# Performance work log

Hardware: AMD Instinct MI355X
Metric: run time of the kernel (lower is better)

## Reference

```python
import jax, jax.numpy as jnp
import numpy as np

KAPPA = 5.0
EPS_NORM = 1e-12  # torch F.normalize eps
EPS_LOG = 1e-09


def setup_inputs() -> dict:
    key = jax.random.key(0)
    student_output = jax.random.normal(key, (16384, 256), dtype=jnp.float32)
    return {"student_output": student_output}


def reference(student_output) -> jnp.ndarray:
    # L2-normalize rows (matches F.normalize: x / max(||x||, eps))
    norm = jnp.linalg.norm(student_output, axis=-1, keepdims=True)
    x_norm = student_output / jnp.maximum(norm, EPS_NORM)
    # pairwise cosine similarity [n, n]
    sim = x_norm @ x_norm.T
    kernel = jnp.exp(KAPPA * sim)
    density_estimates = kernel.sum(axis=1)  # [n]
    entropy = -jnp.mean(jnp.log(density_estimates + EPS_LOG))
    return entropy
```

## Files before the change

### kernel.cpp

```cpp
#include <hip/hip_runtime.h>


#define NROWS 16384
#define KDIM 256
#define NTILE 128
#define NT (NROWS / NTILE)
#define NSTRIP 4
#define TOTAL_BLOCKS (NT * NSTRIP)

#define SQRT_KLOG2E 2.68579577857f

typedef int i32x4_t __attribute__((ext_vector_type(4)));
typedef int i32x8_t __attribute__((ext_vector_type(8)));
typedef float f32x16_t __attribute__((ext_vector_type(16)));
typedef __attribute__((address_space(1))) const void global_cvoid_t;
typedef __attribute__((address_space(3))) void lds_void_t;

#if __has_builtin(__builtin_amdgcn_exp2f)
#define EXP2(x) __builtin_amdgcn_exp2f(x)
#else
#define EXP2(x) exp2f(x)
#endif

union frag8 { i32x8_t v8; i32x4_t v4[2]; };

__global__ __launch_bounds__(256)
void kde_normalize(const float* __restrict__ X, unsigned int* __restrict__ Xn8,
                   float* __restrict__ density, unsigned int* __restrict__ ticket) {
  const int wave = threadIdx.x >> 6;
  const int lane = threadIdx.x & 63;
  const int row = blockIdx.x * 4 + wave;
  const float4 v = ((const float4*)(X + (size_t)row * KDIM))[lane];
  float ss = v.x * v.x + v.y * v.y + v.z * v.z + v.w * v.w;
  ss += __shfl_xor(ss, 1);
  ss += __shfl_xor(ss, 2);
  ss += __shfl_xor(ss, 4);
  ss += __shfl_xor(ss, 8);
  ss += __shfl_xor(ss, 16);
  ss += __shfl_xor(ss, 32);
  const float scale = SQRT_KLOG2E / fmaxf(sqrtf(ss), 1e-12f);
  int p = 0;
  p = __builtin_amdgcn_cvt_pk_fp8_f32(v.x * scale, v.y * scale, p, false);
  p = __builtin_amdgcn_cvt_pk_fp8_f32(v.z * scale, v.w * scale, p, true);
  Xn8[(size_t)row * 64 + lane] = (unsigned int)p;
  if (threadIdx.x < 4) density[blockIdx.x * 4 + threadIdx.x] = 0.0f;
  if (blockIdx.x == 0 && threadIdx.x == 0) *ticket = 0u;
}

__global__ __launch_bounds__(512, 4)
void kde_gemm(const unsigned char* __restrict__ Xn8, float* __restrict__ density,
              unsigned int* __restrict__ ticket, float* __restrict__ out) {
  extern __shared__ char smem[];
  char* buf0 = smem;
  char* buf1 = smem + 32768;

  const int tid = threadIdx.x;
  const int wave = tid >> 6;
  const int lane = tid & 63;
  const int wr = wave >> 1;
  const int wc = wave & 1;
  const int m32 = lane & 31;
  const int h = lane >> 5;
  const int bi = blockIdx.x;
  const int s = blockIdx.y;
  const int t0 = s * 16;
  const int nt = (s == 0 && bi < NT / 2) ? 17 : 16;
  const char* Xb = (const char*)Xn8;

#define STAGE(base_row, dst)                                                      \
  for (int c = wave; c < 32; c += 8) {                                            \
    const int rt = c >> 3, kb = (c >> 1) & 3, hh = c & 1;                         \
    const size_t gofs =                                                           \
        (size_t)((base_row) + rt * 32 + m32) * KDIM + kb * 64 + h * 32 + hh * 16; \
    __builtin_amdgcn_global_load_lds((global_cvoid_t*)(Xb + gofs),                \
                                     (lds_void_t*)((dst) + c * 1024), 16, 0, 0);  \
  }

  STAGE(bi * NTILE, buf0);
  STAGE(((bi + t0) & (NT - 1)) * NTILE, buf1);
  __syncthreads();

  frag8 areg[4];
#pragma unroll
  for (int kb = 0; kb < 4; kb++) {
    const char* pa = buf0 + (wr * 8 + kb * 2) * 1024 + lane * 16;
    areg[kb].v4[0] = *(const i32x4_t*)pa;
    areg[kb].v4[1] = *(const i32x4_t*)(pa + 1024);
  }
  __syncthreads();

  float rs[16];
#pragma unroll
  for (int r = 0; r < 16; r++) rs[r] = 0.0f;

  for (int k = 0; k < nt; ++k) {
    const int t = t0 + (k == 16 ? 48 : k) + (k == 16 ? 16 : 0);
    const int J = (bi + t) & (NT - 1);
    char* rbuf = (k & 1) ? buf0 : buf1;
    char* sbuf = (k & 1) ? buf1 : buf0;

    if (k + 1 < nt) {
      const int tn = t0 + (k + 1 == 16 ? 64 : k + 1);
      STAGE(((bi + tn) & (NT - 1)) * NTILE, sbuf);
    }

    f32x16_t acc[2];
#pragma unroll
    for (int j = 0; j < 2; j++) acc[j] = (f32x16_t)0.0f;

#pragma unroll
    for (int kb = 0; kb < 4; ++kb) {
      frag8 bf[2];
#pragma unroll
      for (int j = 0; j < 2; j++) {
        const char* pb = rbuf + ((wc * 2 + j) * 8 + kb * 2) * 1024 + lane * 16;
        bf[j].v4[0] = *(const i32x4_t*)pb;
        bf[j].v4[1] = *(const i32x4_t*)(pb + 1024);
      }
#pragma unroll
      for (int j = 0; j < 2; j++)
        acc[j] = __builtin_amdgcn_mfma_scale_f32_32x32x64_f8f6f4(
            areg[kb].v8, bf[j].v8, acc[j], 0, 0, 0, 127, 0, 127);
    }

    float cs[2] = {0.0f, 0.0f};
#pragma unroll
    for (int j = 0; j < 2; j++)
#pragma unroll
      for (int r = 0; r < 16; r++) {
        const float e = EXP2(acc[j][r]);
        rs[r] += e;
        cs[j] += e;
      }

    if (t != 0) {
#pragma unroll
      for (int j = 0; j < 2; j++) {
        float v = cs[j] + __shfl_xor(cs[j], 32);
        if (h == 0)
          atomicAdd(&density[J * NTILE + wc * 64 + j * 32 + m32], v);
      }
    }

    __syncthreads();
  }

#pragma unroll
  for (int r = 0; r < 16; r++) {
    float v = rs[r];
    v += __shfl_xor(v, 1);
    v += __shfl_xor(v, 2);
    v += __shfl_xor(v, 4);
    v += __shfl_xor(v, 8);
    v += __shfl_xor(v, 16);
    if (m32 == 0) {
      const int row = bi * NTILE + wr * 32 + (r & 3) + 8 * (r >> 2) + 4 * h;
      atomicAdd(&density[row], v);
    }
  }
#undef STAGE

  __syncthreads();
  if (tid == 0) {
    __threadfence();
    ((volatile unsigned int*)smem)[0] = atomicAdd(ticket, 1u);
  }
  __syncthreads();
  if (((volatile unsigned int*)smem)[0] == TOTAL_BLOCKS - 1) {
    __threadfence();
    float ssum = 0.0f;
    for (int i = tid; i < NROWS; i += 512) {
      const float d = __hip_atomic_load(&density[i], __ATOMIC_RELAXED,
                                        __HIP_MEMORY_SCOPE_AGENT);
      ssum += logf(d + 1e-9f);
    }
    ssum += __shfl_xor(ssum, 1);
    ssum += __shfl_xor(ssum, 2);
    ssum += __shfl_xor(ssum, 4);
    ssum += __shfl_xor(ssum, 8);
    ssum += __shfl_xor(ssum, 16);
    ssum += __shfl_xor(ssum, 32);
    float* red = ((float*)smem) + 16;
    if (lane == 0) red[wave] = ssum;
    __syncthreads();
    if (tid == 0) {
      float tot = 0.0f;
      for (int w = 0; w < 8; w++) tot += red[w];
      out[0] = -tot / (float)NROWS;
    }
  }
}

extern "C" void kernel_launch(void* const* d_in, const int* in_sizes, int n_in,
                              void* d_out, int out_size, void* d_ws, size_t ws_size,
                              hipStream_t stream) {
  const float* X = (const float*)d_in[0];
  float* out = (float*)d_out;
  char* ws = (char*)d_ws;
  unsigned int* Xn8 = (unsigned int*)ws;
  float* density = (float*)(ws + (size_t)NROWS * KDIM);
  unsigned int* ticket = (unsigned int*)(density + NROWS);

  hipFuncSetAttribute((const void*)kde_gemm,
                      hipFuncAttributeMaxDynamicSharedMemorySize, 65536);

  kde_normalize<<<NROWS / 4, 256, 0, stream>>>(X, Xn8, density, ticket);
  kde_gemm<<<dim3(NT, NSTRIP), 512, 65536, stream>>>((const unsigned char*)ws,
                                                     density, ticket, out);
}
```

Baseline: 124.5 us.

## Defer column-sum atomics to an LDS-reduced epilogue and fully unroll tile loop

Per-tile column sums are now stored in registers and written to LDS after the main loop. They are reduced across the four row-waves there, so each column gets one global atomicAdd instead of four per tile. The main 16-tile loop is fully unrolled, and the extra diagonal-symmetric tile is peeled into its own block. This cuts global atomic traffic and keeps atomics out of the pipelined MFMA loop, in exchange for more registers and a larger code body.

Result: slower. 355.5 us (+185.6%).

```diff
diff --git a/kernel.cpp b/kernel.cpp
--- a/kernel.cpp
+++ b/kernel.cpp
@@ -64,7 +64,7 @@
   const int bi = blockIdx.x;
   const int s = blockIdx.y;
   const int t0 = s * 16;
-  const int nt = (s == 0 && bi < NT / 2) ? 17 : 16;
+  const bool extra = (s == 0 && bi < NT / 2);
   const char* Xb = (const char*)Xn8;
 
 #define STAGE(base_row, dst)                                                      \
@@ -92,17 +92,20 @@
   float rs[16];
 #pragma unroll
   for (int r = 0; r < 16; r++) rs[r] = 0.0f;
-
-  for (int k = 0; k < nt; ++k) {
-    const int t = t0 + (k == 16 ? 48 : k) + (k == 16 ? 16 : 0);
-    const int J = (bi + t) & (NT - 1);
+  float cs_save[16];
+
+#pragma unroll
+  for (int k = 0; k < 16; ++k) {
+    const int J = (bi + t0 + k) & (NT - 1);
     char* rbuf = (k & 1) ? buf0 : buf1;
     char* sbuf = (k & 1) ? buf1 : buf0;
 
-    if (k + 1 < nt) {
-      const int tn = t0 + (k + 1 == 16 ? 64 : k + 1);
-      STAGE(((bi + tn) & (NT - 1)) * NTILE, sbuf);
-    }
+    if (k < 15) {
+      STAGE(((bi + t0 + k + 1) & (NT - 1)) * NTILE, sbuf);
+    } else if (extra) {
+      STAGE(((bi + 64) & (NT - 1)) * NTILE, sbuf);
+    }
+    (void)J;
 
     f32x16_t acc[2];
 #pragma unroll
@@ -123,26 +126,77 @@
             areg[kb].v8, bf[j].v8, acc[j], 0, 0, 0, 127, 0, 127);
     }
 
-    float cs[2] = {0.0f, 0.0f};
-#pragma unroll
-    for (int j = 0; j < 2; j++)
-#pragma unroll
-      for (int r = 0; r < 16; r++) {
-        const float e = EXP2(acc[j][r]);
-        rs[r] += e;
-        cs[j] += e;
+    float c0 = 0.0f, c1 = 0.0f;
+#pragma unroll
+    for (int r = 0; r < 16; r++) {
+      const float e0 = EXP2(acc[0][r]);
+      const float e1 = EXP2(acc[1][r]);
+      rs[r] += e0 + e1;
+      c0 += e0;
+      c1 += e1;
+    }
+    c0 += __shfl_xor(c0, 32);
+    c1 += __shfl_xor(c1, 32);
+    cs_save[k] = h ? c1 : c0;
+
+    __syncthreads();
+  }
+
+  if (extra) {
+    const int J = (bi + 64) & (NT - 1);
+    f32x16_t acc[2];
+#pragma unroll
+    for (int j = 0; j < 2; j++) acc[j] = (f32x16_t)0.0f;
+#pragma unroll
+    for (int kb = 0; kb < 4; ++kb) {
+      frag8 bf[2];
+#pragma unroll
+      for (int j = 0; j < 2; j++) {
+        const char* pb = buf1 + ((wc * 2 + j) * 8 + kb * 2) * 1024 + lane * 16;
+        bf[j].v4[0] = *(const i32x4_t*)pb;
+        bf[j].v4[1] = *(const i32x4_t*)(pb + 1024);
       }
-
-    if (t != 0) {
-#pragma unroll
-      for (int j = 0; j < 2; j++) {
-        float v = cs[j] + __shfl_xor(cs[j], 32);
-        if (h == 0)
-          atomicAdd(&density[J * NTILE + wc * 64 + j * 32 + m32], v);
+#pragma unroll
+      for (int j = 0; j < 2; j++)
+        acc[j] = __builtin_amdgcn_mfma_scale_f32_32x32x64_f8f6f4(
+            areg[kb].v8, bf[j].v8, acc[j], 0, 0, 0, 127, 0, 127);
+    }
+    float c0 = 0.0f, c1 = 0.0f;
+#pragma unroll
+    for (int r = 0; r < 16; r++) {
+      const float e0 = EXP2(acc[0][r]);
+      const float e1 = EXP2(acc[1][r]);
+      rs[r] += e0 + e1;
+      c0 += e0;
+      c1 += e1;
+    }
+    c0 += __shfl_xor(c0, 32);
+    c1 += __shfl_xor(c1, 32);
+    if (h == 0) {
+      atomicAdd(&density[J * NTILE + wc * 64 + m32], c0);
+      atomicAdd(&density[J * NTILE + wc * 64 + 32 + m32], c1);
+    }
+  }
+
+  {
+    float* csLds = (float*)buf0;
+#pragma unroll
+    for (int k = 0; k < 16; ++k)
+      csLds[(wr * 16 + k) * 128 + wc * 64 + lane] = cs_save[k];
+    __syncthreads();
+#pragma unroll
+    for (int i = 0; i < 4; ++i) {
+      const int idx = tid + i * 512;
+      const int k = idx >> 7, col = idx & 127;
+      if (s != 0 || k != 0) {
+        const float v = csLds[(0 * 16 + k) * 128 + col] +
+                        csLds[(1 * 16 + k) * 128 + col] +
+                        csLds[(2 * 16 + k) * 128 + col] +
+                        csLds[(3 * 16 + k) * 128 + col];
+        const int J = (bi + t0 + k) & (NT - 1);
+        atomicAdd(&density[J * NTILE + col], v);
       }
     }
-
-    __syncthreads();
   }
 
 #pragma unroll
```

## Drop LDS double buffering and double grid strips for more occupancy

Applied to the files above, without the earlier changes.

Removes the double-buffered LDS prefetch so each block uses 32 KB instead of 64 KB, and stages each column tile synchronously before computing. NSTRIP goes from 4 to 8, doubling the block count and halving the tiles per block (8 or 9 instead of 16 or 17). The aim is more resident blocks and more parallelism so other blocks hide load latency, replacing in-block overlap. The cost is that each block now stalls on its own loads, and the extra blocks add more atomics and more A-tile reloads. The exp accumulation loop is also reordered to interleave the two accumulators.

Measured after the change: 142.5 us. 14.5% more time.

```diff
diff --git a/kernel.cpp b/kernel.cpp
--- a/kernel.cpp
+++ b/kernel.cpp
@@ -5,7 +5,7 @@
 #define KDIM 256
 #define NTILE 128
 #define NT (NROWS / NTILE)
-#define NSTRIP 4
+#define NSTRIP 8
 #define TOTAL_BLOCKS (NT * NSTRIP)
 
 #define SQRT_KLOG2E 2.68579577857f
@@ -51,8 +51,7 @@
 void kde_gemm(const unsigned char* __restrict__ Xn8, float* __restrict__ density,
               unsigned int* __restrict__ ticket, float* __restrict__ out) {
   extern __shared__ char smem[];
-  char* buf0 = smem;
-  char* buf1 = smem + 32768;
+  char* buf = smem;
 
   const int tid = threadIdx.x;
   const int wave = tid >> 6;
@@ -63,27 +62,25 @@
   const int h = lane >> 5;
   const int bi = blockIdx.x;
   const int s = blockIdx.y;
-  const int t0 = s * 16;
-  const int nt = (s == 0 && bi < NT / 2) ? 17 : 16;
+  const int t0 = s * 8;
+  const int nt = (s == 0 && bi < NT / 2) ? 9 : 8;
   const char* Xb = (const char*)Xn8;
 
-#define STAGE(base_row, dst)                                                      \
+#define STAGE(base_row)                                                           \
   for (int c = wave; c < 32; c += 8) {                                            \
     const int rt = c >> 3, kb = (c >> 1) & 3, hh = c & 1;                         \
     const size_t gofs =                                                           \
         (size_t)((base_row) + rt * 32 + m32) * KDIM + kb * 64 + h * 32 + hh * 16; \
     __builtin_amdgcn_global_load_lds((global_cvoid_t*)(Xb + gofs),                \
-                                     (lds_void_t*)((dst) + c * 1024), 16, 0, 0);  \
-  }
-
-  STAGE(bi * NTILE, buf0);
-  STAGE(((bi + t0) & (NT - 1)) * NTILE, buf1);
-  __syncthreads();
-
+                                     (lds_void_t*)(buf + c * 1024), 16, 0, 0);    \
+  }
+
+  STAGE(bi * NTILE);
+  __syncthreads();
   frag8 areg[4];
 #pragma unroll
   for (int kb = 0; kb < 4; kb++) {
-    const char* pa = buf0 + (wr * 8 + kb * 2) * 1024 + lane * 16;
+    const char* pa = buf + (wr * 8 + kb * 2) * 1024 + lane * 16;
     areg[kb].v4[0] = *(const i32x4_t*)pa;
     areg[kb].v4[1] = *(const i32x4_t*)(pa + 1024);
   }
@@ -94,15 +91,11 @@
   for (int r = 0; r < 16; r++) rs[r] = 0.0f;
 
   for (int k = 0; k < nt; ++k) {
-    const int t = t0 + (k == 16 ? 48 : k) + (k == 16 ? 16 : 0);
+    const int t = (k == 8) ? 64 : t0 + k;
     const int J = (bi + t) & (NT - 1);
-    char* rbuf = (k & 1) ? buf0 : buf1;
-    char* sbuf = (k & 1) ? buf1 : buf0;
-
-    if (k + 1 < nt) {
-      const int tn = t0 + (k + 1 == 16 ? 64 : k + 1);
-      STAGE(((bi + tn) & (NT - 1)) * NTILE, sbuf);
-    }
+
+    STAGE(J * NTILE);
+    __syncthreads();
 
     f32x16_t acc[2];
 #pragma unroll
@@ -113,7 +106,7 @@
       frag8 bf[2];
 #pragma unroll
       for (int j = 0; j < 2; j++) {
-        const char* pb = rbuf + ((wc * 2 + j) * 8 + kb * 2) * 1024 + lane * 16;
+        const char* pb = buf + ((wc * 2 + j) * 8 + kb * 2) * 1024 + lane * 16;
         bf[j].v4[0] = *(const i32x4_t*)pb;
         bf[j].v4[1] = *(const i32x4_t*)(pb + 1024);
       }
@@ -123,22 +116,22 @@
             areg[kb].v8, bf[j].v8, acc[j], 0, 0, 0, 127, 0, 127);
     }
 
-    float cs[2] = {0.0f, 0.0f};
-#pragma unroll
-    for (int j = 0; j < 2; j++)
-#pragma unroll
-      for (int r = 0; r < 16; r++) {
-        const float e = EXP2(acc[j][r]);
-        rs[r] += e;
-        cs[j] += e;
-      }
+    float c0 = 0.0f, c1 = 0.0f;
+#pragma unroll
+    for (int r = 0; r < 16; r++) {
+      const float e0 = EXP2(acc[0][r]);
+      const float e1 = EXP2(acc[1][r]);
+      rs[r] += e0 + e1;
+      c0 += e0;
+      c1 += e1;
+    }
 
     if (t != 0) {
-#pragma unroll
-      for (int j = 0; j < 2; j++) {
-        float v = cs[j] + __shfl_xor(cs[j], 32);
-        if (h == 0)
-          atomicAdd(&density[J * NTILE + wc * 64 + j * 32 + m32], v);
+      c0 += __shfl_xor(c0, 32);
+      c1 += __shfl_xor(c1, 32);
+      if (h == 0) {
+        atomicAdd(&density[J * NTILE + wc * 64 + m32], c0);
+        atomicAdd(&density[J * NTILE + wc * 64 + 32 + m32], c1);
       }
     }
 
@@ -202,9 +195,9 @@
   unsigned int* ticket = (unsigned int*)(density + NROWS);
 
   hipFuncSetAttribute((const void*)kde_gemm,
-                      hipFuncAttributeMaxDynamicSharedMemorySize, 65536);
+                      hipFuncAttributeMaxDynamicSharedMemorySize, 32768);
 
   kde_normalize<<<NROWS / 4, 256, 0, stream>>>(X, Xn8, density, ticket);
-  kde_gemm<<<dim3(NT, NSTRIP), 512, 65536, stream>>>((const unsigned char*)ws,
+  kde_gemm<<<dim3(NT, NSTRIP), 512, 32768, stream>>>((const unsigned char*)ws,
                                                      density, ticket, out);
 }
```
